# Kernel optimization log

Measured on AMD Instinct MI355X. Metric: run time of the kernel, lower is better.

Reference implementation:

```python
import jax, jax.numpy as jnp
from jax import lax
import numpy as np

D_MODEL = 1024
D_STATE = 64
D_CONV = 4
EXPAND = 2
HEADDIM = 64
D_INNER = EXPAND * D_MODEL          # 2048
NHEADS = D_INNER // HEADDIM         # 32
CHUNK = 64
CONV_DIM = D_INNER + 2 * D_STATE    # 2176
D_IN_PROJ = 2 * D_INNER + 2 * D_STATE + NHEADS  # 4256
B_SZ = 4
SEQLEN = 2048
EPS = 1e-5


def _silu(x):
    return x * jax.nn.sigmoid(x)


def _segsum(x):
    # x: [..., T]; returns [..., T, T] with [i,j] = sum_{j<k<=i} x[k], -inf above diag
    T = x.shape[-1]
    xe = jnp.broadcast_to(x[..., None], x.shape + (T,))
    strict_lower = jnp.tril(jnp.ones((T, T), bool), -1)
    xe = jnp.where(strict_lower, xe, 0.0)
    s = jnp.cumsum(xe, axis=-2)
    lower = jnp.tril(jnp.ones((T, T), bool), 0)
    return jnp.where(lower, s, -jnp.inf)


def setup_inputs() -> dict:
    key = jax.random.key(0)
    ks = jax.random.split(key, 5)
    u = jax.random.normal(ks[0], (B_SZ, SEQLEN, D_MODEL), jnp.float32)
    W_in = jax.random.normal(ks[1], (D_IN_PROJ, D_MODEL), jnp.float32) * 0.02
    conv_w = jax.random.normal(ks[2], (CONV_DIM, 1, D_CONV), jnp.float32) * 0.2  # depthwise kernel
    conv_b = jnp.zeros((CONV_DIM,), jnp.float32)
    dt_bias = jax.random.uniform(ks[3], (NHEADS,), jnp.float32, -1.0, 1.0)
    A_log = jnp.log(jnp.linspace(1.0, float(NHEADS), NHEADS)).astype(jnp.float32)
    D = jnp.ones((NHEADS,), jnp.float32)
    norm_w = jnp.ones((D_INNER,), jnp.float32)
    W_out = jax.random.normal(ks[4], (D_MODEL, D_INNER), jnp.float32) * 0.02
    return dict(u=u, W_in=W_in, conv_w=conv_w, conv_b=conv_b, dt_bias=dt_bias,
                A_log=A_log, D=D, norm_w=norm_w, W_out=W_out)


def reference(u, W_in, conv_w, conv_b, dt_bias, A_log, D, norm_w, W_out):
    b, s, _ = u.shape
    A = -jnp.exp(A_log)                                   # [H]
    zxbcdt = u @ W_in.T                                   # [b,s,D_IN_PROJ]
    z = zxbcdt[..., :D_INNER]
    xBC = zxbcdt[..., D_INNER:D_INNER + CONV_DIM]
    dt = jax.nn.softplus(zxbcdt[..., D_INNER + CONV_DIM:] + dt_bias)  # [b,s,H]

    # causal depthwise conv1d (left pad d_conv-1 == torch pad-both + slice[:s])
    xc = lax.conv_general_dilated(
        xBC.transpose(0, 2, 1), conv_w, window_strides=(1,),
        padding=[(D_CONV - 1, 0)], feature_group_count=CONV_DIM,
        dimension_numbers=('NCH', 'OIH', 'NCH'))
    xBC = _silu(xc.transpose(0, 2, 1) + conv_b)           # [b,s,CONV_DIM]

    x = xBC[..., :D_INNER].reshape(b, s, NHEADS, HEADDIM)
    Bm = xBC[..., D_INNER:D_INNER + D_STATE]              # [b,s,N]
    Cm = xBC[..., D_INNER + D_STATE:]                     # [b,s,N]

    # SSD chunked scan
    nch = s // CHUNK
    xs = (x * dt[..., None]).reshape(b, nch, CHUNK, NHEADS, HEADDIM)
    Ad = (A * dt).reshape(b, nch, CHUNK, NHEADS)
    Br = Bm.reshape(b, nch, CHUNK, D_STATE)
    Cr = Cm.reshape(b, nch, CHUNK, D_STATE)
    A_ch = Ad.transpose(0, 1, 3, 2)                       # [b,c,h,l]
    A_cum = jnp.cumsum(A_ch, axis=-1)
    L = jnp.exp(_segsum(A_ch))                            # [b,c,h,l,l]
    Y_diag = jnp.einsum('bcln,bcsn,bchls,bcshp->bclhp', Cr, Br, L, xs)
    decay_states = jnp.exp(A_cum[..., -1:] - A_cum)       # [b,c,h,l]
    states = jnp.einsum('bchl,bcln,bclhp->bchpn', decay_states, Br, xs)
    init = jnp.zeros((b, 1, NHEADS, HEADDIM, D_STATE), xs.dtype)
    states = jnp.concatenate([init, states], axis=1)      # [b,c+1,h,p,n]
    total_decay = jnp.pad(A_cum[..., -1].transpose(0, 2, 1), ((0, 0), (0, 0), (1, 0)))
    decay_chunk = jnp.exp(_segsum(total_decay))           # [b,h,c+1,c+1]
    new_states = jnp.einsum('bhzc,bchpn->bzhpn', decay_chunk, states)
    states = new_states[:, :-1]                           # [b,c,h,p,n]
    state_decay_out = jnp.exp(A_cum)
    Y_off = jnp.einsum('bcln,bchpn,bchl->bclhp', Cr, states, state_decay_out)
    y = (Y_diag + Y_off).reshape(b, s, NHEADS, HEADDIM)

    y = y + x * D[:, None]
    y = y.reshape(b, s, D_INNER)
    # gated RMSNorm
    y = y * _silu(z)
    y = y * lax.rsqrt(jnp.mean(y * y, axis=-1, keepdims=True) + EPS) * norm_w
    return y @ W_out.T
```

## Files before the change

### kernel.cpp

```cpp
#include <hip/hip_runtime.h>
#include <hip/hip_bf16.h>

#define BSZ 4
#define SEQ 2048
#define DMODEL 1024
#define DINNER 2048
#define DSTATE 64
#define NH 32
#define HD 64
#define CKL 64
#define NCH 32
#define CONVD 2176
#define DPROJ 4256
#define N1 4224
#define MTOT 8192
#define YSTR 72

typedef __hip_bfloat16 bf16;
typedef __attribute__((ext_vector_type(8))) short short8;
typedef __attribute__((ext_vector_type(4))) short short4_;
typedef __attribute__((ext_vector_type(4))) float f32x4;

__device__ __forceinline__ float sigmoidf_(float x) { return 1.0f / (1.0f + __expf(-x)); }
__device__ __forceinline__ float bits2f(short s) { return __uint_as_float(((unsigned)(unsigned short)s) << 16); }
__device__ __forceinline__ short f2bits(float f) {
    bf16 h = __float2bfloat16(f);
    return *reinterpret_cast<short*>(&h);
}

__device__ __forceinline__ void gl_lds16(const bf16* g, bf16* l) {
    __builtin_amdgcn_global_load_lds((const __attribute__((address_space(1))) void*)g,
                                     (__attribute__((address_space(3))) void*)l, 16, 0, 0);
}

__global__ void k_cvt(const float* __restrict__ src, bf16* __restrict__ dst, int n) {
    int g = (blockIdx.x * 256 + threadIdx.x) * 4;
    if (g < n) {
        f32x4 f = *(const f32x4*)&src[g];
        short4_ o;
#pragma unroll
        for (int j = 0; j < 4; j++) o[j] = f2bits(f[j]);
        *(short4_*)&dst[g] = o;
    }
}

__global__ void k_cvtw(const float* __restrict__ src, const float* __restrict__ nw,
                       bf16* __restrict__ dst, int n) {
    int g = (blockIdx.x * 256 + threadIdx.x) * 4;
    if (g < n) {
        f32x4 f = *(const f32x4*)&src[g];
        f32x4 w = *(const f32x4*)&nw[g & (DINNER - 1)];
        short4_ o;
#pragma unroll
        for (int j = 0; j < 4; j++) o[j] = f2bits(f[j] * w[j]);
        *(short4_*)&dst[g] = o;
    }
}

__global__ __launch_bounds__(256) void k_gemm_bt(const bf16* __restrict__ A, const bf16* __restrict__ W,
                                                 bf16* __restrict__ C, int N, int K, int lda) {
    __shared__ __align__(16) bf16 lA[128 * 64];
    __shared__ __align__(16) bf16 lB[128 * 64];
    const int tid = threadIdx.x;
    const int lane = tid & 63, w = tid >> 6;
    const int wm = w >> 1, wn = w & 1;
    const int lr = lane & 15, lk = lane >> 4;
    const int m0 = blockIdx.y * 128, n0 = blockIdx.x * 128;

    f32x4 acc[4][4];
#pragma unroll
    for (int i = 0; i < 4; i++)
#pragma unroll
        for (int j = 0; j < 4; j++) acc[i][j] = (f32x4){0.f, 0.f, 0.f, 0.f};

    const int r = tid >> 3;
    const int cs = ((tid & 7) ^ (r & 7)) * 8;
    const bf16* ga = A + (size_t)(m0 + r) * lda + cs;
    const bf16* gb = W + (size_t)(n0 + r) * K + cs;
    bf16* la0 = lA + tid * 8;
    bf16* lb0 = lB + tid * 8;
    const int sx = (lr & 7);

    for (int kt = 0; kt < K; kt += 64) {
#pragma unroll
        for (int i = 0; i < 4; i++) {
            gl_lds16(ga + kt + (size_t)(32 * i) * lda, la0 + 2048 * i);
            gl_lds16(gb + kt + (size_t)(32 * i) * K, lb0 + 2048 * i);
        }
        __syncthreads();
#pragma unroll
        for (int hh = 0; hh < 2; hh++) {
            const int cb = ((lk + 4 * hh) ^ sx) * 8;
            short8 af[4], bfr[4];
#pragma unroll
            for (int im = 0; im < 4; im++)
                af[im] = *(const short8*)&lA[(wm * 64 + im * 16 + lr) * 64 + cb];
#pragma unroll
            for (int jn = 0; jn < 4; jn++)
                bfr[jn] = *(const short8*)&lB[(wn * 64 + jn * 16 + lr) * 64 + cb];
#pragma unroll
            for (int im = 0; im < 4; im++)
#pragma unroll
                for (int jn = 0; jn < 4; jn++)
                    acc[im][jn] = __builtin_amdgcn_mfma_f32_16x16x32_bf16(af[im], bfr[jn], acc[im][jn], 0, 0, 0);
        }
        __syncthreads();
    }
#pragma unroll
    for (int im = 0; im < 4; im++) {
        int row = m0 + wm * 64 + im * 16 + lk * 4;
#pragma unroll
        for (int jn = 0; jn < 4; jn++) {
            int col = n0 + wn * 64 + jn * 16 + lr;
            bf16* cp = C + (size_t)row * N + col;
#pragma unroll
            for (int rr = 0; rr < 4; rr++) cp[(size_t)rr * N] = __float2bfloat16(acc[im][jn][rr]);
        }
    }
}

__global__ __launch_bounds__(256) void k_gemm2(const bf16* __restrict__ A, const bf16* __restrict__ W,
                                               const float* __restrict__ rs, float* __restrict__ C) {
    __shared__ __align__(16) bf16 lA[128 * 64];
    __shared__ __align__(16) bf16 lB[64 * 64];
    const int tid = threadIdx.x;
    const int lane = tid & 63, w = tid >> 6;
    const int lr = lane & 15, lk = lane >> 4;
    const int m0 = blockIdx.y * 128, n0 = blockIdx.x * 64;
    const int K = DINNER, N = DMODEL;

    f32x4 acc[2][4];
#pragma unroll
    for (int i = 0; i < 2; i++)
#pragma unroll
        for (int j = 0; j < 4; j++) acc[i][j] = (f32x4){0.f, 0.f, 0.f, 0.f};

    const int r = tid >> 3;
    const int cs = ((tid & 7) ^ (r & 7)) * 8;
    const bf16* ga = A + (size_t)(m0 + r) * N1 + cs;
    const bf16* gb = W + (size_t)(n0 + r) * K + cs;
    bf16* la0 = lA + tid * 8;
    bf16* lb0 = lB + tid * 8;
    const int sx = (lr & 7);

    for (int kt = 0; kt < K; kt += 64) {
#pragma unroll
        for (int i = 0; i < 4; i++)
            gl_lds16(ga + kt + (size_t)(32 * i) * N1, la0 + 2048 * i);
#pragma unroll
        for (int i = 0; i < 2; i++)
            gl_lds16(gb + kt + (size_t)(32 * i) * K, lb0 + 2048 * i);
        __syncthreads();
#pragma unroll
        for (int hh = 0; hh < 2; hh++) {
            const int cb = ((lk + 4 * hh) ^ sx) * 8;
            short8 af[2], bfr[4];
#pragma unroll
            for (int im = 0; im < 2; im++)
                af[im] = *(const short8*)&lA[(w * 32 + im * 16 + lr) * 64 + cb];
#pragma unroll
            for (int jn = 0; jn < 4; jn++)
                bfr[jn] = *(const short8*)&lB[(jn * 16 + lr) * 64 + cb];
#pragma unroll
            for (int im = 0; im < 2; im++)
#pragma unroll
                for (int jn = 0; jn < 4; jn++)
                    acc[im][jn] = __builtin_amdgcn_mfma_f32_16x16x32_bf16(af[im], bfr[jn], acc[im][jn], 0, 0, 0);
        }
        __syncthreads();
    }
#pragma unroll
    for (int im = 0; im < 2; im++) {
        int row = m0 + w * 32 + im * 16 + lk * 4;
#pragma unroll
        for (int rr = 0; rr < 4; rr++) {
            float s = rs[row + rr];
#pragma unroll
            for (int jn = 0; jn < 4; jn++) {
                int col = n0 + jn * 16 + lr;
                C[(size_t)(row + rr) * N + col] = acc[im][jn][rr] * s;
            }
        }
    }
}

__global__ __launch_bounds__(256) void k_rms(const bf16* __restrict__ zx, float* __restrict__ rs) {
    __shared__ float red[4];
    int t = blockIdx.x, tid = threadIdx.x;
    const short* row = (const short*)(zx + (size_t)t * N1);
    short8 v8 = *(const short8*)&row[tid * 8];
    float ss = 0.f;
#pragma unroll
    for (int i = 0; i < 8; i++) { float v = bits2f(v8[i]); ss += v * v; }
#pragma unroll
    for (int d = 32; d > 0; d >>= 1) ss += __shfl_down(ss, d);
    if ((tid & 63) == 0) red[tid >> 6] = ss;
    __syncthreads();
    if (tid == 0)
        rs[t] = rsqrtf((red[0] + red[1] + red[2] + red[3]) * (1.0f / DINNER) + 1e-5f);
}

__global__ __launch_bounds__(256) void k_prep(const float* __restrict__ u, const float* __restrict__ W_in,
                                              const float* __restrict__ dt_bias,
                                              bf16* __restrict__ u_b, float* __restrict__ dtt) {
    __shared__ __align__(16) float us[8 * DMODEL];
    const int t0 = blockIdx.x * 8;
    const int tid = threadIdx.x;
    const float* ur = u + (size_t)t0 * DMODEL;
    bf16* ub = u_b + (size_t)t0 * DMODEL;
#pragma unroll
    for (int i = 0; i < 8; i++) {
        int idx = (i * 256 + tid) * 4;
        f32x4 v = *(const f32x4*)&ur[idx];
        *(f32x4*)&us[idx] = v;
        short4_ o;
#pragma unroll
        for (int j = 0; j < 4; j++) o[j] = f2bits(v[j]);
        *(short4_*)&ub[idx] = o;
    }
    __syncthreads();
    const int h = tid >> 3, sub = tid & 7;
    const float* wr = W_in + (size_t)(DPROJ - NH + h) * DMODEL;
    float s[8] = {};
    for (int k = sub * 4; k < DMODEL; k += 32) {
        f32x4 w4 = *(const f32x4*)&wr[k];
#pragma unroll
        for (int rr = 0; rr < 8; rr++) {
            const float* up = &us[rr * DMODEL + k];
            s[rr] += up[0] * w4[0] + up[1] * w4[1] + up[2] * w4[2] + up[3] * w4[3];
        }
    }
#pragma unroll
    for (int rr = 0; rr < 8; rr++) {
        s[rr] += __shfl_down(s[rr], 4, 8);
        s[rr] += __shfl_down(s[rr], 2, 8);
        s[rr] += __shfl_down(s[rr], 1, 8);
    }
    if (sub == 0) {
        float bh = dt_bias[h];
#pragma unroll
        for (int rr = 0; rr < 8; rr++) {
            float x = s[rr] + bh;
            dtt[(size_t)h * MTOT + t0 + rr] = (x > 20.f) ? x : log1pf(__expf(x));
        }
    }
}

__global__ void k_conv(const bf16* __restrict__ zx, const float* __restrict__ cw,
                       const float* __restrict__ cb, bf16* __restrict__ xbc) {
    int g = (blockIdx.x * 256 + threadIdx.x) * 4;
    if (g >= MTOT * CONVD) return;
    int c0 = g % CONVD;
    int t = g / CONVD;
    int s = t & (SEQ - 1);
    const short* base = (const short*)(zx + (size_t)t * N1 + DINNER + c0);
    f32x4 w0 = *(const f32x4*)&cw[(c0 + 0) * 4];
    f32x4 w1 = *(const f32x4*)&cw[(c0 + 1) * 4];
    f32x4 w2 = *(const f32x4*)&cw[(c0 + 2) * 4];
    f32x4 w3 = *(const f32x4*)&cw[(c0 + 3) * 4];
    f32x4 a = *(const f32x4*)&cb[c0];
#pragma unroll
    for (int k = 0; k < 4; k++) {
        int st = s - 3 + k;
        if (st >= 0) {
            short4_ v = *(const short4_*)(base + (long)(k - 3) * N1);
            a[0] += bits2f(v[0]) * w0[k];
            a[1] += bits2f(v[1]) * w1[k];
            a[2] += bits2f(v[2]) * w2[k];
            a[3] += bits2f(v[3]) * w3[k];
        }
    }
    short4_ o;
#pragma unroll
    for (int j = 0; j < 4; j++) o[j] = f2bits(a[j] * sigmoidf_(a[j]));
    *(short4_*)&xbc[g] = o;
}

__global__ __launch_bounds__(256) void k_ssd(const bf16* __restrict__ xbc, const float* __restrict__ dtt,
                                             const float* __restrict__ A_log, const float* __restrict__ Dp,
                                             bf16* __restrict__ zx) {
    __shared__ __align__(16) short Ct[64 * YSTR];
    __shared__ __align__(16) short Bt[64 * YSTR];
    __shared__ __align__(16) short Bn[64 * YSTR];
    __shared__ __align__(16) short Xt[32 * YSTR];
    __shared__ __align__(16) short Sb[32 * YSTR];
    __shared__ __align__(16) short Gs[4 * 16 * YSTR];
    __shared__ __align__(16) float Sf[32 * 68];
    __shared__ __align__(16) float sdt2[2][64], sAc2[2][64], sf2[2][64];
    __shared__ float set2[2];

    const int ph = blockIdx.x, h = blockIdx.y, b = blockIdx.z;
    const int tid = threadIdx.x;
    const int lane = tid & 63, w = tid >> 6;
    const int lr = lane & 15, lk = lane >> 4;
    const float Ah = -__expf(A_log[h]);
    const float Dh = Dp[h];
    const int xcol = h * HD + ph * 32;

    const int lrow = tid >> 2, c0 = (tid & 3) * 16, px = (tid & 3) * 8;
    const int zl = 16 * w + (lane >> 2), zp = (lane & 3) * 8;

    short8 rC0, rC1, rB0, rB1, rX, rZ;
    float rdt;
    auto load_chunk = [&](int cc) {
        int rows0 = b * SEQ + cc * CKL;
        const short* rp = (const short*)(xbc + (size_t)(rows0 + lrow) * CONVD);
        rC0 = *(const short8*)&rp[DINNER + DSTATE + c0];
        rC1 = *(const short8*)&rp[DINNER + DSTATE + c0 + 8];
        rB0 = *(const short8*)&rp[DINNER + c0];
        rB1 = *(const short8*)&rp[DINNER + c0 + 8];
        rX  = *(const short8*)&rp[xcol + px];
        rZ  = *(const short8*)((const short*)zx + (size_t)(rows0 + zl) * N1 + xcol + zp);
        rdt = dtt[(size_t)h * MTOT + rows0 + lane];
    };

    for (int i = tid; i < 32 * 68; i += 256) Sf[i] = 0.f;
    load_chunk(0);
    if (tid < 64) {
        float dv = rdt;
        float v = Ah * dv;
#pragma unroll
        for (int d = 1; d < 64; d <<= 1) { float o = __shfl_up(v, d); if (tid >= d) v += o; }
        float tot = __shfl(v, 63);
        sdt2[0][tid] = dv; sAc2[0][tid] = v; sf2[0][tid] = __expf(tot - v) * dv;
        if (tid == 63) set2[0] = __expf(tot);
    }
    __syncthreads();

    for (int c = 0; c < NCH; c++) {
        const int par = c & 1;
        const int rows0 = b * SEQ + c * CKL;
        *(short8*)&Ct[lrow * YSTR + c0] = rC0;
        *(short8*)&Ct[lrow * YSTR + c0 + 8] = rC1;
        *(short8*)&Bt[lrow * YSTR + c0] = rB0;
        *(short8*)&Bt[lrow * YSTR + c0 + 8] = rB1;
#pragma unroll
        for (int j = 0; j < 8; j++) {
            Bn[(c0 + j) * YSTR + lrow] = rB0[j];
            Bn[(c0 + 8 + j) * YSTR + lrow] = rB1[j];
            Xt[(px + j) * YSTR + lrow] = rX[j];
        }
        {
            int sp = tid >> 3, sn = (tid & 7) * 8;
            f32x4 a0 = *(const f32x4*)&Sf[sp * 68 + sn];
            f32x4 a1 = *(const f32x4*)&Sf[sp * 68 + sn + 4];
            short8 o;
#pragma unroll
            for (int j = 0; j < 4; j++) { o[j] = f2bits(a0[j]); o[4 + j] = f2bits(a1[j]); }
            *(short8*)&Sb[sp * YSTR + sn] = o;
        }
        __syncthreads();

        float etot = set2[par];
        short8 zcur = rZ;
        if (c + 1 < NCH) load_chunk(c + 1);

        short8 cf0 = *(const short8*)&Ct[(16 * w + lr) * YSTR + lk * 8];
        short8 cf1 = *(const short8*)&Ct[(16 * w + lr) * YSTR + 32 + lk * 8];
        f32x4 acc[2];
#pragma unroll
        for (int t = 0; t < 2; t++) {
            short8 s0 = *(const short8*)&Sb[(16 * t + lr) * YSTR + lk * 8];
            short8 s1 = *(const short8*)&Sb[(16 * t + lr) * YSTR + 32 + lk * 8];
            acc[t] = __builtin_amdgcn_mfma_f32_16x16x32_bf16(cf0, s0, (f32x4){0.f, 0.f, 0.f, 0.f}, 0, 0, 0);
            acc[t] = __builtin_amdgcn_mfma_f32_16x16x32_bf16(cf1, s1, acc[t], 0, 0, 0);
        }
        float sAcl[4], el[4];
#pragma unroll
        for (int rr = 0; rr < 4; rr++) { sAcl[rr] = sAc2[par][16 * w + lk * 4 + rr]; el[rr] = __expf(sAcl[rr]); }
#pragma unroll
        for (int t = 0; t < 2; t++)
#pragma unroll
            for (int rr = 0; rr < 4; rr++) acc[t][rr] *= el[rr];
        short* gw = Gs + w * 16 * YSTR;
#pragma unroll
        for (int t = 0; t < 4; t++) {
            short8 b0 = *(const short8*)&Bt[(16 * t + lr) * YSTR + lk * 8];
            short8 b1 = *(const short8*)&Bt[(16 * t + lr) * YSTR + 32 + lk * 8];
            f32x4 g = __builtin_amdgcn_mfma_f32_16x16x32_bf16(cf0, b0, (f32x4){0.f, 0.f, 0.f, 0.f}, 0, 0, 0);
            g = __builtin_amdgcn_mfma_f32_16x16x32_bf16(cf1, b1, g, 0, 0, 0);
            int s = 16 * t + lr;
            float sAcs = sAc2[par][s], dts = sdt2[par][s];
#pragma unroll
            for (int rr = 0; rr < 4; rr++) {
                int l = 16 * w + lk * 4 + rr;
                float v = (s <= l) ? g[rr] * __expf(sAcl[rr] - sAcs) * dts : 0.f;
                gw[(lk * 4 + rr) * YSTR + s] = f2bits(v);
            }
        }
        short8 gf0 = *(const short8*)&gw[lr * YSTR + lk * 8];
        short8 gf1 = *(const short8*)&gw[lr * YSTR + 32 + lk * 8];
#pragma unroll
        for (int t = 0; t < 2; t++) {
            short8 x0 = *(const short8*)&Xt[(16 * t + lr) * YSTR + lk * 8];
            short8 x1 = *(const short8*)&Xt[(16 * t + lr) * YSTR + 32 + lk * 8];
            acc[t] = __builtin_amdgcn_mfma_f32_16x16x32_bf16(gf0, x0, acc[t], 0, 0, 0);
            acc[t] = __builtin_amdgcn_mfma_f32_16x16x32_bf16(gf1, x1, acc[t], 0, 0, 0);
        }
        {
            int pw = w & 1, nh2 = w >> 1;
            short8 xt0 = *(const short8*)&Xt[(16 * pw + lr) * YSTR + lk * 8];
            short8 xt1 = *(const short8*)&Xt[(16 * pw + lr) * YSTR + 32 + lk * 8];
            f32x4 sa0 = *(const f32x4*)&sf2[par][lk * 8];
            f32x4 sa1 = *(const f32x4*)&sf2[par][lk * 8 + 4];
            f32x4 sb0 = *(const f32x4*)&sf2[par][32 + lk * 8];
            f32x4 sb1 = *(const f32x4*)&sf2[par][32 + lk * 8 + 4];
            short8 xd0, xd1;
#pragma unroll
            for (int j = 0; j < 4; j++) {
                xd0[j]     = f2bits(bits2f(xt0[j])     * sa0[j]);
                xd0[4 + j] = f2bits(bits2f(xt0[4 + j]) * sa1[j]);
                xd1[j]     = f2bits(bits2f(xt1[j])     * sb0[j]);
                xd1[4 + j] = f2bits(bits2f(xt1[4 + j]) * sb1[j]);
            }
#pragma unroll
            for (int j = 0; j < 2; j++) {
                int nt = 2 * nh2 + j;
                short8 b0 = *(const short8*)&Bn[(16 * nt + lr) * YSTR + lk * 8];
                short8 b1 = *(const short8*)&Bn[(16 * nt + lr) * YSTR + 32 + lk * 8];
                f32x4 sacc = __builtin_amdgcn_mfma_f32_16x16x32_bf16(xd0, b0, (f32x4){0.f, 0.f, 0.f, 0.f}, 0, 0, 0);
                sacc = __builtin_amdgcn_mfma_f32_16x16x32_bf16(xd1, b1, sacc, 0, 0, 0);
#pragma unroll
                for (int rr = 0; rr < 4; rr++) {
                    int n = 16 * nt + lr;
                    int p = 16 * pw + lk * 4 + rr;
                    Sf[p * 68 + n] = Sf[p * 68 + n] * etot + sacc[rr];
                }
            }
        }
#pragma unroll
        for (int t = 0; t < 2; t++) {
#pragma unroll
            for (int rr = 0; rr < 4; rr++) {
                int p = 16 * t + lr;
                int l = 16 * w + lk * 4 + rr;
                float y = acc[t][rr] + Dh * bits2f(Xt[p * YSTR + l]);
                Ct[l * YSTR + p] = f2bits(y);
            }
        }
        {
            short8 y8 = *(const short8*)&Ct[zl * YSTR + zp];
            short* zpp = (short*)zx + (size_t)(rows0 + zl) * N1 + xcol + zp;
            short8 o;
#pragma unroll
            for (int j = 0; j < 8; j++) {
                float z = bits2f(zcur[j]);
                o[j] = f2bits(bits2f(y8[j]) * (z * sigmoidf_(z)));
            }
            *(short8*)zpp = o;
        }
        if (c + 1 < NCH && tid < 64) {
            int p2 = (c + 1) & 1;
            float dv = rdt;
            float v = Ah * dv;
#pragma unroll
            for (int d = 1; d < 64; d <<= 1) { float o = __shfl_up(v, d); if (tid >= d) v += o; }
            float tot = __shfl(v, 63);
            sdt2[p2][tid] = dv; sAc2[p2][tid] = v; sf2[p2][tid] = __expf(tot - v) * dv;
            if (tid == 63) set2[p2] = __expf(tot);
        }
        __syncthreads();
    }
}

extern "C" void kernel_launch(void* const* d_in, const int* in_sizes, int n_in,
                              void* d_out, int out_size, void* d_ws, size_t ws_size,
                              hipStream_t stream) {
    const float* u       = (const float*)d_in[0];
    const float* W_in    = (const float*)d_in[1];
    const float* conv_w  = (const float*)d_in[2];
    const float* conv_b  = (const float*)d_in[3];
    const float* dt_bias = (const float*)d_in[4];
    const float* A_log   = (const float*)d_in[5];
    const float* Dp      = (const float*)d_in[6];
    const float* norm_w  = (const float*)d_in[7];
    const float* W_out   = (const float*)d_in[8];
    float* out = (float*)d_out;

    char* ws = (char*)d_ws;
    bf16* zx     = (bf16*)ws;  ws += (size_t)MTOT * N1 * 2;
    bf16* xbc    = (bf16*)ws;  ws += (size_t)MTOT * CONVD * 2;
    bf16* wout_b = (bf16*)ws;  ws += (size_t)DMODEL * DINNER * 2;
    float* dtt   = (float*)ws; ws += (size_t)NH * MTOT * 4;
    float* rsb   = (float*)ws; ws += (size_t)MTOT * 4;

    bf16* u_b   = (bf16*)d_out;
    bf16* win_b = (bf16*)((char*)d_out + (size_t)MTOT * DMODEL * 2);

    k_prep<<<MTOT / 8, 256, 0, stream>>>(u, W_in, dt_bias, u_b, dtt);
    k_cvt<<<(N1 * DMODEL / 4 + 255) / 256, 256, 0, stream>>>(W_in, win_b, N1 * DMODEL);
    k_cvtw<<<(DMODEL * DINNER / 4 + 255) / 256, 256, 0, stream>>>(W_out, norm_w, wout_b, DMODEL * DINNER);

    k_gemm_bt<<<dim3(N1 / 128, MTOT / 128), 256, 0, stream>>>(u_b, win_b, zx, N1, DMODEL, DMODEL);

    k_conv<<<(MTOT * CONVD / 4 + 255) / 256, 256, 0, stream>>>(zx, conv_w, conv_b, xbc);

    k_ssd<<<dim3(2, NH, BSZ), 256, 0, stream>>>(xbc, dtt, A_log, Dp, zx);

    k_rms<<<MTOT, 256, 0, stream>>>(zx, rsb);

    k_gemm2<<<dim3(DMODEL / 64, MTOT / 128), 256, 0, stream>>>(zx, wout_b, rsb, out);
}
```

Before: 405.8 us.

## Fuse RMS norm into output GEMM, merge weight casts, double-buffer SSD LDS

Drops the separate RMS-norm kernel. The output GEMM now accumulates each row's sum of squares from the A fragments it already loads, then reduces it through shuffles and shared memory before scaling. The two weight-conversion kernels are merged into one launch. The SSD kernel double-buffers its chunk tiles in LDS and scatters the next chunk and its dt scan after compute, which removes one barrier per chunk. The costs are extra VALU work in the GEMM inner loop, twice the SSD LDS footprint (which may lower occupancy), and redundant sum-of-squares work across the N-tile blocks.

```diff
diff --git a/kernel.cpp b/kernel.cpp
--- a/kernel.cpp
+++ b/kernel.cpp
@@ -33,27 +33,24 @@
                                      (__attribute__((address_space(3))) void*)l, 16, 0, 0);
 }
 
-__global__ void k_cvt(const float* __restrict__ src, bf16* __restrict__ dst, int n) {
+__global__ void k_cvt2(const float* __restrict__ W_in, const float* __restrict__ W_out,
+                       const float* __restrict__ nw, bf16* __restrict__ win_b,
+                       bf16* __restrict__ wout_b) {
     int g = (blockIdx.x * 256 + threadIdx.x) * 4;
-    if (g < n) {
-        f32x4 f = *(const f32x4*)&src[g];
+    if (g < N1 * DMODEL) {
+        f32x4 f = *(const f32x4*)&W_in[g];
         short4_ o;
 #pragma unroll
         for (int j = 0; j < 4; j++) o[j] = f2bits(f[j]);
-        *(short4_*)&dst[g] = o;
-    }
-}
-
-__global__ void k_cvtw(const float* __restrict__ src, const float* __restrict__ nw,
-                       bf16* __restrict__ dst, int n) {
-    int g = (blockIdx.x * 256 + threadIdx.x) * 4;
-    if (g < n) {
-        f32x4 f = *(const f32x4*)&src[g];
-        f32x4 w = *(const f32x4*)&nw[g & (DINNER - 1)];
+        *(short4_*)&win_b[g] = o;
+    } else if (g < N1 * DMODEL + DMODEL * DINNER) {
+        int g2 = g - N1 * DMODEL;
+        f32x4 f = *(const f32x4*)&W_out[g2];
+        f32x4 w = *(const f32x4*)&nw[g2 & (DINNER - 1)];
         short4_ o;
 #pragma unroll
         for (int j = 0; j < 4; j++) o[j] = f2bits(f[j] * w[j]);
-        *(short4_*)&dst[g] = o;
+        *(short4_*)&wout_b[g2] = o;
     }
 }
 
@@ -120,9 +117,10 @@
 }
 
 __global__ __launch_bounds__(256) void k_gemm2(const bf16* __restrict__ A, const bf16* __restrict__ W,
-                                               const float* __restrict__ rs, float* __restrict__ C) {
+                                               float* __restrict__ C) {
     __shared__ __align__(16) bf16 lA[128 * 64];
     __shared__ __align__(16) bf16 lB[64 * 64];
+    __shared__ float rsrow[128];
     const int tid = threadIdx.x;
     const int lane = tid & 63, w = tid >> 6;
     const int lr = lane & 15, lk = lane >> 4;
@@ -134,6 +132,7 @@
     for (int i = 0; i < 2; i++)
 #pragma unroll
         for (int j = 0; j < 4; j++) acc[i][j] = (f32x4){0.f, 0.f, 0.f, 0.f};
+    float ssq[2] = {0.f, 0.f};
 
     const int r = tid >> 3;
     const int cs = ((tid & 7) ^ (r & 7)) * 8;
@@ -156,8 +155,11 @@
             const int cb = ((lk + 4 * hh) ^ sx) * 8;
             short8 af[2], bfr[4];
 #pragma unroll
-            for (int im = 0; im < 2; im++)
+            for (int im = 0; im < 2; im++) {
                 af[im] = *(const short8*)&lA[(w * 32 + im * 16 + lr) * 64 + cb];
+#pragma unroll
+                for (int j = 0; j < 8; j++) { float v = bits2f(af[im][j]); ssq[im] += v * v; }
+            }
 #pragma unroll
             for (int jn = 0; jn < 4; jn++)
                 bfr[jn] = *(const short8*)&lB[(jn * 16 + lr) * 64 + cb];
@@ -171,10 +173,19 @@
     }
 #pragma unroll
     for (int im = 0; im < 2; im++) {
-        int row = m0 + w * 32 + im * 16 + lk * 4;
+        float s = ssq[im];
+        s += __shfl_down(s, 32);
+        s += __shfl_down(s, 16);
+        if (lane < 16) rsrow[w * 32 + im * 16 + lane] = rsqrtf(s * (1.0f / DINNER) + 1e-5f);
+    }
+    __syncthreads();
+#pragma unroll
+    for (int im = 0; im < 2; im++) {
+        int rloc = w * 32 + im * 16 + lk * 4;
+        int row = m0 + rloc;
 #pragma unroll
         for (int rr = 0; rr < 4; rr++) {
-            float s = rs[row + rr];
+            float s = rsrow[rloc + rr];
 #pragma unroll
             for (int jn = 0; jn < 4; jn++) {
                 int col = n0 + jn * 16 + lr;
@@ -182,22 +193,6 @@
             }
         }
     }
-}
-
-__global__ __launch_bounds__(256) void k_rms(const bf16* __restrict__ zx, float* __restrict__ rs) {
-    __shared__ float red[4];
-    int t = blockIdx.x, tid = threadIdx.x;
-    const short* row = (const short*)(zx + (size_t)t * N1);
-    short8 v8 = *(const short8*)&row[tid * 8];
-    float ss = 0.f;
-#pragma unroll
-    for (int i = 0; i < 8; i++) { float v = bits2f(v8[i]); ss += v * v; }
-#pragma unroll
-    for (int d = 32; d > 0; d >>= 1) ss += __shfl_down(ss, d);
-    if ((tid & 63) == 0) red[tid >> 6] = ss;
-    __syncthreads();
-    if (tid == 0)
-        rs[t] = rsqrtf((red[0] + red[1] + red[2] + red[3]) * (1.0f / DINNER) + 1e-5f);
 }
 
 __global__ __launch_bounds__(256) void k_prep(const float* __restrict__ u, const float* __restrict__ W_in,
@@ -279,11 +274,11 @@
 __global__ __launch_bounds__(256) void k_ssd(const bf16* __restrict__ xbc, const float* __restrict__ dtt,
                                              const float* __restrict__ A_log, const float* __restrict__ Dp,
                                              bf16* __restrict__ zx) {
-    __shared__ __align__(16) short Ct[64 * YSTR];
-    __shared__ __align__(16) short Bt[64 * YSTR];
-    __shared__ __align__(16) short Bn[64 * YSTR];
-    __shared__ __align__(16) short Xt[32 * YSTR];
-    __shared__ __align__(16) short Sb[32 * YSTR];
+    __shared__ __align__(16) short Ct[2][64 * YSTR];
+    __shared__ __align__(16) short Bt[2][64 * YSTR];
+    __shared__ __align__(16) short Bn[2][64 * YSTR];
+    __shared__ __align__(16) short Xt[2][32 * YSTR];
+    __shared__ __align__(16) short Sb[2][32 * YSTR];
     __shared__ __align__(16) short Gs[4 * 16 * YSTR];
     __shared__ __align__(16) float Sf[32 * 68];
     __shared__ __align__(16) float sdt2[2][64], sAc2[2][64], sf2[2][64];
@@ -313,55 +308,51 @@
         rZ  = *(const short8*)((const short*)zx + (size_t)(rows0 + zl) * N1 + xcol + zp);
         rdt = dtt[(size_t)h * MTOT + rows0 + lane];
     };
+    auto scatter = [&](int buf) {
+        *(short8*)&Ct[buf][lrow * YSTR + c0] = rC0;
+        *(short8*)&Ct[buf][lrow * YSTR + c0 + 8] = rC1;
+        *(short8*)&Bt[buf][lrow * YSTR + c0] = rB0;
+        *(short8*)&Bt[buf][lrow * YSTR + c0 + 8] = rB1;
+#pragma unroll
+        for (int j = 0; j < 8; j++) {
+            Bn[buf][(c0 + j) * YSTR + lrow] = rB0[j];
+            Bn[buf][(c0 + 8 + j) * YSTR + lrow] = rB1[j];
+            Xt[buf][(px + j) * YSTR + lrow] = rX[j];
+        }
+    };
+    auto dtscan = [&](int buf) {
+        if (tid < 64) {
+            float dv = rdt;
+            float v = Ah * dv;
+#pragma unroll
+            for (int d = 1; d < 64; d <<= 1) { float o = __shfl_up(v, d); if (tid >= d) v += o; }
+            float tot = __shfl(v, 63);
+            sdt2[buf][tid] = dv; sAc2[buf][tid] = v; sf2[buf][tid] = __expf(tot - v) * dv;
+            if (tid == 63) set2[buf] = __expf(tot);
+        }
+    };
 
     for (int i = tid; i < 32 * 68; i += 256) Sf[i] = 0.f;
+    for (int i = tid; i < 32 * YSTR; i += 256) Sb[0][i] = 0;
     load_chunk(0);
-    if (tid < 64) {
-        float dv = rdt;
-        float v = Ah * dv;
-#pragma unroll
-        for (int d = 1; d < 64; d <<= 1) { float o = __shfl_up(v, d); if (tid >= d) v += o; }
-        float tot = __shfl(v, 63);
-        sdt2[0][tid] = dv; sAc2[0][tid] = v; sf2[0][tid] = __expf(tot - v) * dv;
-        if (tid == 63) set2[0] = __expf(tot);
-    }
+    scatter(0);
+    dtscan(0);
     __syncthreads();
 
     for (int c = 0; c < NCH; c++) {
-        const int par = c & 1;
+        const int par = c & 1, nb = par ^ 1;
         const int rows0 = b * SEQ + c * CKL;
-        *(short8*)&Ct[lrow * YSTR + c0] = rC0;
-        *(short8*)&Ct[lrow * YSTR + c0 + 8] = rC1;
-        *(short8*)&Bt[lrow * YSTR + c0] = rB0;
-        *(short8*)&Bt[lrow * YSTR + c0 + 8] = rB1;
-#pragma unroll
-        for (int j = 0; j < 8; j++) {
-            Bn[(c0 + j) * YSTR + lrow] = rB0[j];
-            Bn[(c0 + 8 + j) * YSTR + lrow] = rB1[j];
-            Xt[(px + j) * YSTR + lrow] = rX[j];
-        }
-        {
-            int sp = tid >> 3, sn = (tid & 7) * 8;
-            f32x4 a0 = *(const f32x4*)&Sf[sp * 68 + sn];
-            f32x4 a1 = *(const f32x4*)&Sf[sp * 68 + sn + 4];
-            short8 o;
-#pragma unroll
-            for (int j = 0; j < 4; j++) { o[j] = f2bits(a0[j]); o[4 + j] = f2bits(a1[j]); }
-            *(short8*)&Sb[sp * YSTR + sn] = o;
-        }
-        __syncthreads();
-
         float etot = set2[par];
         short8 zcur = rZ;
         if (c + 1 < NCH) load_chunk(c + 1);
 
-        short8 cf0 = *(const short8*)&Ct[(16 * w + lr) * YSTR + lk * 8];
-        short8 cf1 = *(const short8*)&Ct[(16 * w + lr) * YSTR + 32 + lk * 8];
+        short8 cf0 = *(const short8*)&Ct[par][(16 * w + lr) * YSTR + lk * 8];
+        short8 cf1 = *(const short8*)&Ct[par][(16 * w + lr) * YSTR + 32 + lk * 8];
         f32x4 acc[2];
 #pragma unroll
         for (int t = 0; t < 2; t++) {
-            short8 s0 = *(const short8*)&Sb[(16 * t + lr) * YSTR + lk * 8];
-            short8 s1 = *(const short8*)&Sb[(16 * t + lr) * YSTR + 32 + lk * 8];
+            short8 s0 = *(const short8*)&Sb[par][(16 * t + lr) * YSTR + lk * 8];
+            short8 s1 = *(const short8*)&Sb[par][(16 * t + lr) * YSTR + 32 + lk * 8];
             acc[t] = __builtin_amdgcn_mfma_f32_16x16x32_bf16(cf0, s0, (f32x4){0.f, 0.f, 0.f, 0.f}, 0, 0, 0);
             acc[t] = __builtin_amdgcn_mfma_f32_16x16x32_bf16(cf1, s1, acc[t], 0, 0, 0);
         }
@@ -375,8 +366,8 @@
         short* gw = Gs + w * 16 * YSTR;
 #pragma unroll
         for (int t = 0; t < 4; t++) {
-            short8 b0 = *(const short8*)&Bt[(16 * t + lr) * YSTR + lk * 8];
-            short8 b1 = *(const short8*)&Bt[(16 * t + lr) * YSTR + 32 + lk * 8];
+            short8 b0 = *(const short8*)&Bt[par][(16 * t + lr) * YSTR + lk * 8];
+            short8 b1 = *(const short8*)&Bt[par][(16 * t + lr) * YSTR + 32 + lk * 8];
             f32x4 g = __builtin_amdgcn_mfma_f32_16x16x32_bf16(cf0, b0, (f32x4){0.f, 0.f, 0.f, 0.f}, 0, 0, 0);
             g = __builtin_amdgcn_mfma_f32_16x16x32_bf16(cf1, b1, g, 0, 0, 0);
             int s = 16 * t + lr;
@@ -392,15 +383,15 @@
         short8 gf1 = *(const short8*)&gw[lr * YSTR + 32 + lk * 8];
 #pragma unroll
         for (int t = 0; t < 2; t++) {
-            short8 x0 = *(const short8*)&Xt[(16 * t + lr) * YSTR + lk * 8];
-            short8 x1 = *(const short8*)&Xt[(16 * t + lr) * YSTR + 32 + lk * 8];
+            short8 x0 = *(const short8*)&Xt[par][(16 * t + lr) * YSTR + lk * 8];
+            short8 x1 = *(const short8*)&Xt[par][(16 * t + lr) * YSTR + 32 + lk * 8];
             acc[t] = __builtin_amdgcn_mfma_f32_16x16x32_bf16(gf0, x0, acc[t], 0, 0, 0);
             acc[t] = __builtin_amdgcn_mfma_f32_16x16x32_bf16(gf1, x1, acc[t], 0, 0, 0);
         }
         {
             int pw = w & 1, nh2 = w >> 1;
-            short8 xt0 = *(const short8*)&Xt[(16 * pw + lr) * YSTR + lk * 8];
-            short8 xt1 = *(const short8*)&Xt[(16 * pw + lr) * YSTR + 32 + lk * 8];
+            short8 xt0 = *(const short8*)&Xt[par][(16 * pw + lr) * YSTR + lk * 8];
+            short8 xt1 = *(const short8*)&Xt[par][(16 * pw + lr) * YSTR + 32 + lk * 8];
             f32x4 sa0 = *(const f32x4*)&sf2[par][lk * 8];
             f32x4 sa1 = *(const f32x4*)&sf2[par][lk * 8 + 4];
             f32x4 sb0 = *(const f32x4*)&sf2[par][32 + lk * 8];
@@ -416,15 +407,17 @@
 #pragma unroll
             for (int j = 0; j < 2; j++) {
                 int nt = 2 * nh2 + j;
-                short8 b0 = *(const short8*)&Bn[(16 * nt + lr) * YSTR + lk * 8];
-                short8 b1 = *(const short8*)&Bn[(16 * nt + lr) * YSTR + 32 + lk * 8];
+                short8 b0 = *(const short8*)&Bn[par][(16 * nt + lr) * YSTR + lk * 8];
+                short8 b1 = *(const short8*)&Bn[par][(16 * nt + lr) * YSTR + 32 + lk * 8];
                 f32x4 sacc = __builtin_amdgcn_mfma_f32_16x16x32_bf16(xd0, b0, (f32x4){0.f, 0.f, 0.f, 0.f}, 0, 0, 0);
                 sacc = __builtin_amdgcn_mfma_f32_16x16x32_bf16(xd1, b1, sacc, 0, 0, 0);
 #pragma unroll
                 for (int rr = 0; rr < 4; rr++) {
                     int n = 16 * nt + lr;
                     int p = 16 * pw + lk * 4 + rr;
-                    Sf[p * 68 + n] = Sf[p * 68 + n] * etot + sacc[rr];
+                    float nv = Sf[p * 68 + n] * etot + sacc[rr];
+                    Sf[p * 68 + n] = nv;
+                    Sb[nb][p * YSTR + n] = f2bits(nv);
                 }
             }
         }
@@ -434,12 +427,12 @@
             for (int rr = 0; rr < 4; rr++) {
                 int p = 16 * t + lr;
                 int l = 16 * w + lk * 4 + rr;
-                float y = acc[t][rr] + Dh * bits2f(Xt[p * YSTR + l]);
-                Ct[l * YSTR + p] = f2bits(y);
+                float y = acc[t][rr] + Dh * bits2f(Xt[par][p * YSTR + l]);
+                Ct[par][l * YSTR + p] = f2bits(y);
             }
         }
         {
-            short8 y8 = *(const short8*)&Ct[zl * YSTR + zp];
+            short8 y8 = *(const short8*)&Ct[par][zl * YSTR + zp];
             short* zpp = (short*)zx + (size_t)(rows0 + zl) * N1 + xcol + zp;
             short8 o;
 #pragma unroll
@@ -449,15 +442,9 @@
             }
             *(short8*)zpp = o;
         }
-        if (c + 1 < NCH && tid < 64) {
-            int p2 = (c + 1) & 1;
-            float dv = rdt;
-            float v = Ah * dv;
-#pragma unroll
-            for (int d = 1; d < 64; d <<= 1) { float o = __shfl_up(v, d); if (tid >= d) v += o; }
-            float tot = __shfl(v, 63);
-            sdt2[p2][tid] = dv; sAc2[p2][tid] = v; sf2[p2][tid] = __expf(tot - v) * dv;
-            if (tid == 63) set2[p2] = __expf(tot);
+        if (c + 1 < NCH) {
+            scatter(nb);
+            dtscan(nb);
         }
         __syncthreads();
     }
@@ -482,14 +469,13 @@
     bf16* xbc    = (bf16*)ws;  ws += (size_t)MTOT * CONVD * 2;
     bf16* wout_b = (bf16*)ws;  ws += (size_t)DMODEL * DINNER * 2;
     float* dtt   = (float*)ws; ws += (size_t)NH * MTOT * 4;
-    float* rsb   = (float*)ws; ws += (size_t)MTOT * 4;
 
     bf16* u_b   = (bf16*)d_out;
     bf16* win_b = (bf16*)((char*)d_out + (size_t)MTOT * DMODEL * 2);
 
     k_prep<<<MTOT / 8, 256, 0, stream>>>(u, W_in, dt_bias, u_b, dtt);
-    k_cvt<<<(N1 * DMODEL / 4 + 255) / 256, 256, 0, stream>>>(W_in, win_b, N1 * DMODEL);
-    k_cvtw<<<(DMODEL * DINNER / 4 + 255) / 256, 256, 0, stream>>>(W_out, norm_w, wout_b, DMODEL * DINNER);
+    k_cvt2<<<((N1 * DMODEL + DMODEL * DINNER) / 4 + 255) / 256, 256, 0, stream>>>(
+        W_in, W_out, norm_w, win_b, wout_b);
 
     k_gemm_bt<<<dim3(N1 / 128, MTOT / 128), 256, 0, stream>>>(u_b, win_b, zx, N1, DMODEL, DMODEL);
 
@@ -497,7 +483,5 @@
 
     k_ssd<<<dim3(2, NH, BSZ), 256, 0, stream>>>(xbc, dtt, A_log, Dp, zx);
 
-    k_rms<<<MTOT, 256, 0, stream>>>(zx, rsb);
-
-    k_gemm2<<<dim3(DMODEL / 64, MTOT / 128), 256, 0, stream>>>(zx, wout_b, rsb, out);
-}
+    k_gemm2<<<dim3(DMODEL / 64, MTOT / 128), 256, 0, stream>>>(zx, wout_b, out);
+}
```

After: 405.3 us. No clear change (-0.1%).
